# Kernel tuning notes

Hardware: AMD Instinct MI355X
Metric: run time of the kernel (lower is better)

Reference implementation:

```python
import jax, jax.numpy as jnp
import numpy as np

CODEBOOK_SIZE = 8192
D_MODEL = 256
COMMITMENT_COST = 0.25


def setup_inputs() -> dict:
    key = jax.random.key(0)
    k1, k2 = jax.random.split(key)
    z = jax.random.normal(k1, (16, 512, D_MODEL), dtype=jnp.float32)
    # uniform(-1/K, 1/K) init like the torch module
    codebook = jax.random.uniform(
        k2, (CODEBOOK_SIZE, D_MODEL), dtype=jnp.float32,
        minval=-1.0 / CODEBOOK_SIZE, maxval=1.0 / CODEBOOK_SIZE)
    return {"z": z, "codebook": codebook}


def reference(z, codebook):
    B, P, D = z.shape
    flat = z.reshape(-1, D)  # [N, D]
    distances = (jnp.sum(flat * flat, axis=1, keepdims=True)
                 + jnp.sum(codebook * codebook, axis=1)
                 - 2.0 * jnp.matmul(flat, codebook.T))
    indices = jnp.argmin(distances, axis=1)  # [N] int
    quantized = codebook[indices]            # [N, D] gather
    # non-EMA VQ loss: codebook loss + commitment loss
    e_latent_loss = jnp.mean((jax.lax.stop_gradient(quantized) - flat) ** 2)
    q_latent_loss = jnp.mean((quantized - jax.lax.stop_gradient(flat)) ** 2)
    loss = q_latent_loss + COMMITMENT_COST * e_latent_loss
    # straight-through estimator
    quantized_st = flat + jax.lax.stop_gradient(quantized - flat)
    return (loss, quantized_st.reshape(B, P, D), indices.reshape(B, P))
```

## Files before the change

### kernel.cpp

```cpp
#include <hip/hip_runtime.h>
#include <hip/hip_bf16.h>
#include <math.h>


#define NROWS 8192
#define DDIM  256
#define KCW   8192
#define CAP   64
#define MARGIN 6e-4f
#define TILES 32

typedef __attribute__((ext_vector_type(8))) short short8;
typedef __attribute__((ext_vector_type(4))) float f32x4;
typedef unsigned int u32;

__device__ inline void async_copy16(void* lds_uniform, const void* gsrc) {
  __builtin_amdgcn_global_load_lds(
      (const __attribute__((address_space(1))) u32*)gsrc,
      (__attribute__((address_space(3))) u32*)lds_uniform, 16, 0, 0);
}

__device__ inline unsigned fmap(float f) {
  unsigned b = __float_as_uint(f);
  return (b & 0x80000000u) ? ~b : (b | 0x80000000u);
}
__device__ inline float funmap(unsigned u) {
  unsigned b = (u & 0x80000000u) ? (u & 0x7FFFFFFFu) : ~u;
  return __uint_as_float(b);
}

__global__ __launch_bounds__(256) void k_prep_cast(const float* __restrict__ z,
                                                   const float* __restrict__ cb,
                                                   ushort* __restrict__ zb,
                                                   ushort* __restrict__ cbb,
                                                   float* __restrict__ e2f,
                                                   unsigned* __restrict__ cnt) {
  int t = threadIdx.x, w = t >> 6, lane = t & 63;
  int wid = blockIdx.x * 4 + w;
  bool isCb = wid >= NROWS;
  int row = isCb ? wid - NROWS : wid;
  const float* src = (isCb ? cb : z) + (size_t)row * DDIM + lane * 4;
  float4 v = *reinterpret_cast<const float4*>(src);
  ushort4 o;
  __hip_bfloat16 bx = __float2bfloat16(v.x); o.x = *(ushort*)&bx;
  __hip_bfloat16 by = __float2bfloat16(v.y); o.y = *(ushort*)&by;
  __hip_bfloat16 bz = __float2bfloat16(v.z); o.z = *(ushort*)&bz;
  __hip_bfloat16 bw = __float2bfloat16(v.w); o.w = *(ushort*)&bw;
  ushort* dst = (isCb ? cbb : zb) + (size_t)row * DDIM + lane * 4;
  *reinterpret_cast<ushort4*>(dst) = o;
  if (isCb) {
    double d = (double)v.x * v.x + (double)v.y * v.y + (double)v.z * v.z + (double)v.w * v.w;
#pragma unroll
    for (int off = 1; off < 64; off <<= 1) d += __shfl_xor(d, off);
    if (lane == 0) e2f[row] = (float)d;
  } else {
    if (lane == 0) cnt[row] = 0;
  }
}

__global__ __launch_bounds__(256, 2) void k_sweep(const ushort* __restrict__ zb,
                                                  const ushort* __restrict__ cbb,
                                                  const float* __restrict__ e2f,
                                                  unsigned* __restrict__ cnt,
                                                  int* __restrict__ cand) {
  __shared__ ushort Bb[128 * 256];
  __shared__ unsigned runmin[32];
  int t = threadIdx.x, w = t >> 6, lane = t & 63;
  int wg = ((blockIdx.x & 7) << 6) | (blockIdx.x >> 3);
  int rt = wg >> 1, h = wg & 1;
  int R0 = rt * 32;
  int C0 = h * 4096;
  int cl = lane & 15, g = lane >> 4;

  if (t < 32) runmin[t] = ~0u;

  short8 Areg[2][8];
#pragma unroll
  for (int m = 0; m < 2; ++m)
#pragma unroll
    for (int kk = 0; kk < 8; ++kk)
      Areg[m][kk] = *reinterpret_cast<const short8*>(
          &zb[(size_t)(R0 + m * 16 + cl) * DDIM + kk * 32 + g * 8]);
  __syncthreads();

  for (int tile = 0; tile < TILES; ++tile) {
    int CT = C0 + tile * 128;
#pragma unroll
    for (int i = 0; i < 16; ++i) {
      int col = i * 8 + w * 2 + (lane >> 5);
      const ushort* src = cbb + (size_t)(CT + col) * DDIM + ((lane & 31) ^ (col & 7)) * 8;
      char* dst = (char*)Bb + i * 4096 + w * 1024;
      async_copy16(dst, src);
    }
    float e2v[2];
#pragma unroll
    for (int n = 0; n < 2; ++n) e2v[n] = e2f[CT + w * 32 + n * 16 + cl];
    __syncthreads();

    f32x4 acc[2][2];
#pragma unroll
    for (int m = 0; m < 2; ++m)
#pragma unroll
      for (int n = 0; n < 2; ++n) acc[m][n] = (f32x4){0.f, 0.f, 0.f, 0.f};
#pragma unroll
    for (int kk = 0; kk < 8; ++kk) {
      short8 bfrag[2];
#pragma unroll
      for (int n = 0; n < 2; ++n) {
        int col = w * 32 + n * 16 + cl;
        int addr = col * 512 + (((kk * 4 + g) ^ (col & 7)) << 4);
        bfrag[n] = *reinterpret_cast<const short8*>((char*)Bb + addr);
      }
#pragma unroll
      for (int m = 0; m < 2; ++m)
#pragma unroll
        for (int n = 0; n < 2; ++n)
          acc[m][n] = __builtin_amdgcn_mfma_f32_16x16x32_bf16(Areg[m][kk], bfrag[n], acc[m][n], 0, 0, 0);
    }

    float sc[2][2][4];
#pragma unroll
    for (int m = 0; m < 2; ++m)
#pragma unroll
      for (int n = 0; n < 2; ++n)
#pragma unroll
        for (int j = 0; j < 4; ++j)
          sc[m][n][j] = __fsub_rn(e2v[n], __fmul_rn(2.0f, acc[m][n][j]));

#pragma unroll
    for (int m = 0; m < 2; ++m)
#pragma unroll
      for (int j = 0; j < 4; ++j) {
        float mn = fminf(sc[m][0][j], sc[m][1][j]);
#pragma unroll
        for (int off = 1; off < 16; off <<= 1) mn = fminf(mn, __shfl_xor(mn, off));
        if (cl == 0) atomicMin(&runmin[m * 16 + g * 4 + j], fmap(mn));
      }
#pragma unroll
    for (int m = 0; m < 2; ++m)
#pragma unroll
      for (int j = 0; j < 4; ++j) {
        int rloc = m * 16 + g * 4 + j;
        float thr = funmap(runmin[rloc]) + MARGIN;
#pragma unroll
        for (int n = 0; n < 2; ++n) {
          if (sc[m][n][j] <= thr) {
            int row = R0 + rloc;
            unsigned slot = atomicAdd(&cnt[row], 1u);
            if (slot < CAP) cand[row * CAP + slot] = CT + w * 32 + n * 16 + cl;
          }
        }
      }
    __syncthreads();
  }
}

__global__ __launch_bounds__(256) void k_rescore_gather(const float* __restrict__ z,
                                                        const float* __restrict__ cb,
                                                        const float* __restrict__ e2f,
                                                        const unsigned* __restrict__ cnt,
                                                        const int* __restrict__ cand,
                                                        float* __restrict__ out_q,
                                                        float* __restrict__ out_idx,
                                                        float* __restrict__ lpart) {
  int t = threadIdx.x, w = t >> 6, lane = t & 63;
  int row = blockIdx.x * 4 + w;
  const float* xp = z + (size_t)row * DDIM;
  float4 x4 = *reinterpret_cast<const float4*>(xp + lane * 4);
  double rd = (double)x4.x * x4.x + (double)x4.y * x4.y + (double)x4.z * x4.z + (double)x4.w * x4.w;
#pragma unroll
  for (int off = 1; off < 64; off <<= 1) rd += __shfl_xor(rd, off);
  float r2v = (float)rd;

  unsigned n = cnt[row];
  float s = INFINITY; int ci = 0x7fffffff;
  if (n <= CAP) {
    if (lane < (int)n) {
      ci = cand[row * CAP + lane];
      const float* ep = cb + (size_t)ci * DDIM;
      float acc = 0.f;
      for (int k = 0; k < DDIM; ++k) acc = __fmaf_rn(xp[k], ep[k], acc);
      s = __fsub_rn(__fadd_rn(r2v, e2f[ci]), __fmul_rn(2.0f, acc));
    }
  } else {
    for (int base = 0; base < KCW; base += 64) {
      int c = base + lane;
      const float* ep = cb + (size_t)c * DDIM;
      float acc = 0.f;
      for (int k = 0; k < DDIM; ++k) acc = __fmaf_rn(xp[k], ep[k], acc);
      float scv = __fsub_rn(__fadd_rn(r2v, e2f[c]), __fmul_rn(2.0f, acc));
      if (scv < s) { s = scv; ci = c; }
    }
  }
#pragma unroll
  for (int off = 1; off < 64; off <<= 1) {
    float os = __shfl_xor(s, off); int oi = __shfl_xor(ci, off);
    if (os < s || (os == s && oi < ci)) { s = os; ci = oi; }
  }
  if (lane == 0) out_idx[row] = (float)ci;

  float4 q = *reinterpret_cast<const float4*>(cb + (size_t)ci * DDIM + lane * 4);
  float* o = out_q + (size_t)row * DDIM + lane * 4;
  o[0] = q.x; o[1] = q.y; o[2] = q.z; o[3] = q.w;
  float dx = q.x - x4.x, dy = q.y - x4.y, dz = q.z - x4.z, dw = q.w - x4.w;
  double d = (double)dx * dx + (double)dy * dy + (double)dz * dz + (double)dw * dw;
#pragma unroll
  for (int off = 1; off < 64; off <<= 1) d += __shfl_xor(d, off);
  if (lane == 0) lpart[row] = (float)d;
}

__global__ __launch_bounds__(256) void k_loss(const float* __restrict__ lpart,
                                              float* __restrict__ out0) {
  __shared__ double red[256];
  int t = threadIdx.x;
  double s = 0.0;
  for (int j = t; j < NROWS; j += 256) s += lpart[j];
  red[t] = s;
  __syncthreads();
  for (int off = 128; off > 0; off >>= 1) {
    if (t < off) red[t] += red[t + off];
    __syncthreads();
  }
  if (t == 0) out0[0] = (float)(1.25 * red[0] / (double)((size_t)NROWS * DDIM));
}

extern "C" void kernel_launch(void* const* d_in, const int* in_sizes, int n_in,
                              void* d_out, int out_size, void* d_ws, size_t ws_size,
                              hipStream_t stream) {
  const float* z  = (const float*)d_in[0];
  const float* cb = (const float*)d_in[1];
  float* out = (float*)d_out;
  char* ws = (char*)d_ws;
  const size_t HALF = (size_t)NROWS * DDIM;

  ushort* zb  = (ushort*)(out + 4);
  ushort* cbb = zb + HALF;

  size_t off = 0;
  float*    e2f   = (float*)(ws + off);    off += NROWS * 4;
  unsigned* cnt   = (unsigned*)(ws + off); off += NROWS * 4;
  float*    lpart = (float*)(ws + off);    off += NROWS * 4;
  int*      cand  = (int*)(ws + off);      off += (size_t)NROWS * CAP * 4;

  float* out_q   = out + 1;
  float* out_idx = out + 1 + HALF;

  k_prep_cast     <<<(2 * NROWS) / 4, 256, 0, stream>>>(z, cb, zb, cbb, e2f, cnt);
  k_sweep         <<<512,             256, 0, stream>>>(zb, cbb, e2f, cnt, cand);
  k_rescore_gather<<<NROWS / 4,       256, 0, stream>>>(z, cb, e2f, cnt, cand, out_q, out_idx, lpart);
  k_loss          <<<1,               256, 0, stream>>>(lpart, out);
}
```

Measured before the change: 220.6 us.

## Retile distance sweep to 128-row blocks with double-buffered codebook tiles

Each sweep block now covers 128 query rows and 1024 codewords instead of 32 rows and 4096 codewords, using 8 waves arranged 4x2. Each codebook tile loaded into LDS is therefore reused by four times as many rows. Codebook tiles are double-buffered, so the next tile's async load overlaps the current tile's MFMA work. Candidate indices are stored as 16-bit values and the candidate cap is doubled, with the rescore loop updated to scan up to two candidates per lane. In exchange, each row's running minimum only spans a 1024-column slice, so more candidates may pass the margin filter and rescoring may cost more.

```diff
diff --git a/kernel.cpp b/kernel.cpp
--- a/kernel.cpp
+++ b/kernel.cpp
@@ -6,9 +6,9 @@
 #define NROWS 8192
 #define DDIM  256
 #define KCW   8192
-#define CAP   64
+#define CAP   128
 #define MARGIN 6e-4f
-#define TILES 32
+#define TILES 16
 
 typedef __attribute__((ext_vector_type(8))) short short8;
 typedef __attribute__((ext_vector_type(4))) float f32x4;
@@ -58,21 +58,21 @@
   }
 }
 
-__global__ __launch_bounds__(256, 2) void k_sweep(const ushort* __restrict__ zb,
+__global__ __launch_bounds__(512, 2) void k_sweep(const ushort* __restrict__ zb,
                                                   const ushort* __restrict__ cbb,
                                                   const float* __restrict__ e2f,
                                                   unsigned* __restrict__ cnt,
-                                                  int* __restrict__ cand) {
-  __shared__ ushort Bb[128 * 256];
-  __shared__ unsigned runmin[32];
+                                                  ushort* __restrict__ cand) {
+  __shared__ ushort Bb[2][64 * 256];
+  __shared__ unsigned runmin[128];
   int t = threadIdx.x, w = t >> 6, lane = t & 63;
   int wg = ((blockIdx.x & 7) << 6) | (blockIdx.x >> 3);
-  int rt = wg >> 1, h = wg & 1;
-  int R0 = rt * 32;
-  int C0 = h * 4096;
+  int rt = wg >> 3, q = wg & 7;
+  int R0 = rt * 128, C0 = q * 1024;
+  int wm = w >> 1, wn = w & 1;
   int cl = lane & 15, g = lane >> 4;
 
-  if (t < 32) runmin[t] = ~0u;
+  if (t < 128) runmin[t] = ~0u;
 
   short8 Areg[2][8];
 #pragma unroll
@@ -80,22 +80,33 @@
 #pragma unroll
     for (int kk = 0; kk < 8; ++kk)
       Areg[m][kk] = *reinterpret_cast<const short8*>(
-          &zb[(size_t)(R0 + m * 16 + cl) * DDIM + kk * 32 + g * 8]);
+          &zb[(size_t)(R0 + wm * 32 + m * 16 + cl) * DDIM + kk * 32 + g * 8]);
+
+#pragma unroll
+  for (int i = 0; i < 4; ++i) {
+    int chunk = i * 8 + w;
+    int col = chunk * 2 + (lane >> 5);
+    const ushort* src = cbb + (size_t)(C0 + col) * DDIM + ((lane & 31) ^ (col & 7)) * 8;
+    async_copy16((char*)Bb[0] + chunk * 1024, src);
+  }
   __syncthreads();
 
   for (int tile = 0; tile < TILES; ++tile) {
-    int CT = C0 + tile * 128;
-#pragma unroll
-    for (int i = 0; i < 16; ++i) {
-      int col = i * 8 + w * 2 + (lane >> 5);
-      const ushort* src = cbb + (size_t)(CT + col) * DDIM + ((lane & 31) ^ (col & 7)) * 8;
-      char* dst = (char*)Bb + i * 4096 + w * 1024;
-      async_copy16(dst, src);
-    }
+    int cur = tile & 1;
+    if (tile + 1 < TILES) {
+      int CTn = C0 + (tile + 1) * 64;
+#pragma unroll
+      for (int i = 0; i < 4; ++i) {
+        int chunk = i * 8 + w;
+        int col = chunk * 2 + (lane >> 5);
+        const ushort* src = cbb + (size_t)(CTn + col) * DDIM + ((lane & 31) ^ (col & 7)) * 8;
+        async_copy16((char*)Bb[cur ^ 1] + chunk * 1024, src);
+      }
+    }
+    int CT = C0 + tile * 64;
     float e2v[2];
 #pragma unroll
-    for (int n = 0; n < 2; ++n) e2v[n] = e2f[CT + w * 32 + n * 16 + cl];
-    __syncthreads();
+    for (int n = 0; n < 2; ++n) e2v[n] = e2f[CT + wn * 32 + n * 16 + cl];
 
     f32x4 acc[2][2];
 #pragma unroll
@@ -107,9 +118,9 @@
       short8 bfrag[2];
 #pragma unroll
       for (int n = 0; n < 2; ++n) {
-        int col = w * 32 + n * 16 + cl;
+        int col = wn * 32 + n * 16 + cl;
         int addr = col * 512 + (((kk * 4 + g) ^ (col & 7)) << 4);
-        bfrag[n] = *reinterpret_cast<const short8*>((char*)Bb + addr);
+        bfrag[n] = *reinterpret_cast<const short8*>((char*)Bb[cur] + addr);
       }
 #pragma unroll
       for (int m = 0; m < 2; ++m)
@@ -134,20 +145,21 @@
         float mn = fminf(sc[m][0][j], sc[m][1][j]);
 #pragma unroll
         for (int off = 1; off < 16; off <<= 1) mn = fminf(mn, __shfl_xor(mn, off));
-        if (cl == 0) atomicMin(&runmin[m * 16 + g * 4 + j], fmap(mn));
-      }
+        if (cl == 0) atomicMin(&runmin[wm * 32 + m * 16 + g * 4 + j], fmap(mn));
+      }
+    int rmv = (int)runmin[wm * 32 + (lane & 31)];
 #pragma unroll
     for (int m = 0; m < 2; ++m)
 #pragma unroll
       for (int j = 0; j < 4; ++j) {
         int rloc = m * 16 + g * 4 + j;
-        float thr = funmap(runmin[rloc]) + MARGIN;
+        float thr = funmap((unsigned)__shfl(rmv, rloc)) + MARGIN;
 #pragma unroll
         for (int n = 0; n < 2; ++n) {
           if (sc[m][n][j] <= thr) {
-            int row = R0 + rloc;
+            int row = R0 + wm * 32 + rloc;
             unsigned slot = atomicAdd(&cnt[row], 1u);
-            if (slot < CAP) cand[row * CAP + slot] = CT + w * 32 + n * 16 + cl;
+            if (slot < CAP) cand[(size_t)row * CAP + slot] = (ushort)(CT + wn * 32 + n * 16 + cl);
           }
         }
       }
@@ -159,7 +171,7 @@
                                                         const float* __restrict__ cb,
                                                         const float* __restrict__ e2f,
                                                         const unsigned* __restrict__ cnt,
-                                                        const int* __restrict__ cand,
+                                                        const ushort* __restrict__ cand,
                                                         float* __restrict__ out_q,
                                                         float* __restrict__ out_idx,
                                                         float* __restrict__ lpart) {
@@ -175,12 +187,17 @@
   unsigned n = cnt[row];
   float s = INFINITY; int ci = 0x7fffffff;
   if (n <= CAP) {
-    if (lane < (int)n) {
-      ci = cand[row * CAP + lane];
-      const float* ep = cb + (size_t)ci * DDIM;
-      float acc = 0.f;
-      for (int k = 0; k < DDIM; ++k) acc = __fmaf_rn(xp[k], ep[k], acc);
-      s = __fsub_rn(__fadd_rn(r2v, e2f[ci]), __fmul_rn(2.0f, acc));
+#pragma unroll
+    for (int base = 0; base < CAP; base += 64) {
+      int k_i = base + lane;
+      if (k_i < (int)n) {
+        int c = cand[(size_t)row * CAP + k_i];
+        const float* ep = cb + (size_t)c * DDIM;
+        float acc = 0.f;
+        for (int k = 0; k < DDIM; ++k) acc = __fmaf_rn(xp[k], ep[k], acc);
+        float scv = __fsub_rn(__fadd_rn(r2v, e2f[c]), __fmul_rn(2.0f, acc));
+        if (scv < s || (scv == s && c < ci)) { s = scv; ci = c; }
+      }
     }
   } else {
     for (int base = 0; base < KCW; base += 64) {
@@ -199,10 +216,10 @@
   }
   if (lane == 0) out_idx[row] = (float)ci;
 
-  float4 q = *reinterpret_cast<const float4*>(cb + (size_t)ci * DDIM + lane * 4);
+  float4 qv = *reinterpret_cast<const float4*>(cb + (size_t)ci * DDIM + lane * 4);
   float* o = out_q + (size_t)row * DDIM + lane * 4;
-  o[0] = q.x; o[1] = q.y; o[2] = q.z; o[3] = q.w;
-  float dx = q.x - x4.x, dy = q.y - x4.y, dz = q.z - x4.z, dw = q.w - x4.w;
+  o[0] = qv.x; o[1] = qv.y; o[2] = qv.z; o[3] = qv.w;
+  float dx = qv.x - x4.x, dy = qv.y - x4.y, dz = qv.z - x4.z, dw = qv.w - x4.w;
   double d = (double)dx * dx + (double)dy * dy + (double)dz * dz + (double)dw * dw;
 #pragma unroll
   for (int off = 1; off < 64; off <<= 1) d += __shfl_xor(d, off);
@@ -240,13 +257,13 @@
   float*    e2f   = (float*)(ws + off);    off += NROWS * 4;
   unsigned* cnt   = (unsigned*)(ws + off); off += NROWS * 4;
   float*    lpart = (float*)(ws + off);    off += NROWS * 4;
-  int*      cand  = (int*)(ws + off);      off += (size_t)NROWS * CAP * 4;
+  ushort*   cand  = (ushort*)(ws + off);   off += (size_t)NROWS * CAP * 2;
 
   float* out_q   = out + 1;
   float* out_idx = out + 1 + HALF;
 
   k_prep_cast     <<<(2 * NROWS) / 4, 256, 0, stream>>>(z, cb, zb, cbb, e2f, cnt);
-  k_sweep         <<<512,             256, 0, stream>>>(zb, cbb, e2f, cnt, cand);
+  k_sweep         <<<512,             512, 0, stream>>>(zb, cbb, e2f, cnt, cand);
   k_rescore_gather<<<NROWS / 4,       256, 0, stream>>>(z, cb, e2f, cnt, cand, out_q, out_idx, lpart);
   k_loss          <<<1,               256, 0, stream>>>(lpart, out);
 }
```

Result: slower. 299.6 us (+35.8%).
